# Kernel optimization log

Measured on AMD Instinct MI355X. Metric: run time of the kernel, lower is better.

Reference implementation:

```python
import jax, jax.numpy as jnp
import numpy as np

B, N, M = 8, 1024, 1024
D, H, P = 256, 4, 128
C = D // H  # per-head dim = 64


def setup_inputs() -> dict:
    key = jax.random.key(0)
    ks = jax.random.split(key, 12)
    s = 1.0 / np.sqrt(D)
    return {
        "input_q": jax.random.normal(ks[0], (B, N, D), jnp.float32),
        "input_k": jax.random.normal(ks[1], (B, M, D), jnp.float32),
        "input_v": jax.random.normal(ks[2], (B, M, D), jnp.float32),
        "Wq": jax.random.normal(ks[3], (D, D), jnp.float32) * s,
        "bq": jnp.zeros((D,), jnp.float32),
        "Wk": jax.random.normal(ks[4], (D, D), jnp.float32) * s,
        "bk": jnp.zeros((D,), jnp.float32),
        "Wv": jax.random.normal(ks[5], (D, D), jnp.float32) * s,
        "bv": jnp.zeros((D,), jnp.float32),
        "emb_table": jax.random.normal(ks[6], (P, D), jnp.float32) * s,
        "attention_factors": jax.random.uniform(ks[7], (B, N, M), jnp.float32),
        "emb_indices_qk": jax.random.randint(ks[8], (B, N, M), 0, P, jnp.int32),
        "key_masks": jnp.zeros((B, M), jnp.bool_),
    }


def _split_heads(x):
    # (B, L, D) -> (B, H, L, C)
    b, l, _ = x.shape
    return x.reshape(b, l, H, C).transpose(0, 2, 1, 3)


def reference(input_q, input_k, input_v, Wq, bq, Wk, bk, Wv, bv,
              emb_table, attention_factors, emb_indices_qk, key_masks):
    q = _split_heads(input_q @ Wq.T + bq)  # (B,H,N,C)
    k = _split_heads(input_k @ Wk.T + bk)  # (B,H,M,C)
    v = _split_heads(input_v @ Wv.T + bv)  # (B,H,M,C)

    # embedding bank: (P, D) -> (H, P, C)   ['p (h c) -> h p c']
    emb_bank = emb_table.reshape(P, H, C).transpose(1, 0, 2)
    scores_p_all = jnp.einsum('bhnc,hpc->bhnp', q, emb_bank)  # (B,H,N,P)
    idx = jnp.broadcast_to(emb_indices_qk[:, None], (q.shape[0], H) + emb_indices_qk.shape[1:])
    scores_p = jnp.take_along_axis(scores_p_all, idx, axis=-1)  # (B,H,N,M)

    scores_e = jnp.einsum('bhnc,bhmc->bhnm', q, k)
    scores = (scores_e + scores_p) / jnp.sqrt(jnp.float32(C))
    scores = attention_factors[:, None] * scores
    scores = jnp.where(key_masks[:, None, None, :], -jnp.inf, scores)
    attn = jax.nn.softmax(scores, axis=-1)  # (B,H,N,M)

    hidden = jnp.einsum('bhnm,bhmc->bhnc', attn, v)
    b, h, n, c = hidden.shape
    hidden = hidden.transpose(0, 2, 1, 3).reshape(b, n, h * c)  # (B,N,D)
    return hidden, attn
```

## Files before the change

kernel.cpp:

```cpp
#include <hip/hip_runtime.h>
#include <math.h>

#define Bb 8
#define Nn 1024
#define Mm 1024
#define Dd 256
#define Hh 4
#define Pp 128

using f16x8 = __attribute__((ext_vector_type(8))) _Float16;
using f32x4 = __attribute__((ext_vector_type(4))) float;
using i32x4 = __attribute__((ext_vector_type(4))) int;

#define MFMA16(a, b, c) __builtin_amdgcn_mfma_f32_16x16x32_f16(a, b, c, 0, 0, 0)

__device__ __forceinline__ int swz(int row, int colByte) {
    return row * 128 + (colByte ^ ((row & 7) << 4));
}

__device__ __forceinline__ void stage8_f32(const float* __restrict__ g, unsigned char* dst) {
    f32x4 a = *(const f32x4*)g;
    f32x4 b = *(const f32x4*)(g + 4);
    f16x8 h;
    h[0] = (_Float16)a[0]; h[1] = (_Float16)a[1]; h[2] = (_Float16)a[2]; h[3] = (_Float16)a[3];
    h[4] = (_Float16)b[0]; h[5] = (_Float16)b[1]; h[6] = (_Float16)b[2]; h[7] = (_Float16)b[3];
    *(f16x8*)dst = h;
}

__global__ __launch_bounds__(256) void proj_kernel(
    const float* __restrict__ xq, const float* __restrict__ xk, const float* __restrict__ xv,
    const float* __restrict__ wq, const float* __restrict__ wk, const float* __restrict__ wv,
    const float* __restrict__ bq, const float* __restrict__ bk, const float* __restrict__ bv,
    _Float16* __restrict__ Qo, _Float16* __restrict__ Ko, _Float16* __restrict__ Vt)
{
    __shared__ __align__(16) unsigned char smem[16384];
    unsigned char* aT = smem;
    unsigned char* bT = smem + 8192;

    const int z = blockIdx.z;
    const float* X    = (z == 0) ? xq : (z == 1) ? xk : xv;
    const float* W    = (z == 0) ? wq : (z == 1) ? wk : wv;
    const float* bias = (z == 0) ? bq : (z == 1) ? bk : bv;

    const int r0 = blockIdx.x * 64;
    const int c0 = blockIdx.y * 64;
    const int l = threadIdx.x;
    const int lane = l & 63;
    const int wx = l >> 6;
    const int grp = lane >> 4, col16 = lane & 15;

    f32x4 acc[4] = {};

    for (int kc = 0; kc < 4; ++kc) {
        for (int it = 0; it < 2; ++it) {
            int s = l + it * 256;
            int row = s >> 3, sl = s & 7;
            stage8_f32(X + (size_t)(r0 + row) * Dd + kc * 64 + sl * 8, aT + swz(row, sl * 16));
            stage8_f32(W + (size_t)(c0 + row) * Dd + kc * 64 + sl * 8, bT + swz(row, sl * 16));
        }
        __syncthreads();
        const int arow = wx * 16 + col16;
        f16x8 af0 = *(const f16x8*)(aT + swz(arow, grp * 16));
        f16x8 af1 = *(const f16x8*)(aT + swz(arow, grp * 16 + 64));
#pragma unroll
        for (int t = 0; t < 4; ++t) {
            int brow = t * 16 + col16;
            f16x8 bf0 = *(const f16x8*)(bT + swz(brow, grp * 16));
            f16x8 bf1 = *(const f16x8*)(bT + swz(brow, grp * 16 + 64));
            acc[t] = MFMA16(af0, bf0, acc[t]);
            acc[t] = MFMA16(af1, bf1, acc[t]);
        }
        __syncthreads();
    }

    if (z < 2) {
        _Float16* O = (z == 0) ? Qo : Ko;
        const float osc = (z == 0) ? 0.125f : 1.0f;
#pragma unroll
        for (int t = 0; t < 4; ++t) {
            float bsc = bias[c0 + t * 16 + col16];
#pragma unroll
            for (int j = 0; j < 4; ++j) {
                int r = r0 + wx * 16 + grp * 4 + j;
                O[(size_t)r * Dd + c0 + t * 16 + col16] = (_Float16)((acc[t][j] + bsc) * osc);
            }
        }
    } else {
        _Float16* vt = (_Float16*)smem;
        __syncthreads();
#pragma unroll
        for (int t = 0; t < 4; ++t) {
            float bsc = bias[c0 + t * 16 + col16];
#pragma unroll
            for (int j = 0; j < 4; ++j) {
                int r = wx * 16 + grp * 4 + j;
                int c = t * 16 + col16;
                vt[c * 72 + r] = (_Float16)(acc[t][j] + bsc);
            }
        }
        __syncthreads();
        const int bo = r0 >> 10, m0 = r0 & 1023, h = blockIdx.y;
        for (int it = 0; it < 2; ++it) {
            int s = l + it * 256;
            int c = s >> 3, m8 = s & 7;
            i32x4 val = *(const i32x4*)(vt + c * 72 + m8 * 8);
            *(i32x4*)(Vt + (size_t)((bo * Hh + h) * 64 + c) * Mm + m0 + m8 * 8) = val;
        }
    }
}

__global__ __launch_bounds__(256) void attn_kernel(
    const _Float16* __restrict__ Qi, const _Float16* __restrict__ Ki,
    const _Float16* __restrict__ Vt, const float* __restrict__ emb,
    const float* __restrict__ afac, const int* __restrict__ eidx,
    const unsigned char* __restrict__ kmask,
    float* __restrict__ hid, float* __restrict__ attn)
{
    __shared__ __align__(16) unsigned char smem[63744];
    unsigned char* Uk = smem;
    unsigned char* Uv = smem + 8192;
    unsigned char* Up = smem + 16384;
    _Float16*      spL = (_Float16*)(smem + 24576);
    float*         afT = (float*)(smem + 41984);
    unsigned char* eiT = smem + 59392;

    const int n0 = blockIdx.x * 64;
    const int h = blockIdx.y, b = blockIdx.z;
    const int l = threadIdx.x, lane = l & 63, wx = l >> 6;
    const int grp = lane >> 4, col16 = lane & 15;

    for (int it = 0; it < 2; ++it) {
        int s = l + it * 256, row = s >> 3, sl = s & 7;
        i32x4 v = *(const i32x4*)(Qi + (size_t)(b * Nn + n0 + row) * Dd + h * 64 + sl * 8);
        *(i32x4*)(Uk + swz(row, sl * 16)) = v;
    }
    for (int it = 0; it < 4; ++it) {
        int s = l + it * 256, p = s >> 3, sl = s & 7;
        unsigned char* dst = (p < 64) ? (Uv + swz(p, sl * 16)) : (Up + swz(p - 64, sl * 16));
        stage8_f32(emb + (size_t)p * Dd + h * 64 + sl * 8, dst);
    }
    __syncthreads();

    const int qrow = wx * 16 + col16;
    f16x8 qf0 = *(const f16x8*)(Uk + swz(qrow, grp * 16));
    f16x8 qf1 = *(const f16x8*)(Uk + swz(qrow, grp * 16 + 64));

#pragma unroll
    for (int t = 0; t < 8; ++t) {
        int prow = t * 16 + col16;
        const unsigned char* base = (t < 4) ? Uv : Up;
        int pr = (t < 4) ? prow : prow - 64;
        f16x8 e0 = *(const f16x8*)(base + swz(pr, grp * 16));
        f16x8 e1 = *(const f16x8*)(base + swz(pr, grp * 16 + 64));
        f32x4 a = {};
        a = MFMA16(qf0, e0, a);
        a = MFMA16(qf1, e1, a);
#pragma unroll
        for (int j = 0; j < 4; ++j)
            spL[(wx * 16 + grp * 4 + j) * 136 + t * 16 + col16] = (_Float16)a[j];
    }
    __syncthreads();

    const size_t afrow0 = (size_t)b * Nn * Mm + (size_t)n0 * Mm;
    const _Float16* Kb = Ki + (size_t)b * Mm * Dd + h * 64;
    const _Float16* Vb = Vt + (size_t)((b * Hh + h) * 64) * Mm;

    float sum_[4] = {0.f, 0.f, 0.f, 0.f};

    for (int mt = 0; mt < 16; ++mt) {
        for (int it = 0; it < 2; ++it) {
            int s = l + it * 256, row = s >> 3, sl = s & 7;
            i32x4 v = *(const i32x4*)(Kb + (size_t)(mt * 64 + row) * Dd + sl * 8);
            *(i32x4*)(Uk + swz(row, sl * 16)) = v;
        }
        for (int it = 0; it < 4; ++it) {
            int s = l + it * 256, row = s >> 4, q4 = s & 15;
            size_t g = afrow0 + (size_t)row * Mm + mt * 64 + q4 * 4;
            f32x4 av = *(const f32x4*)(afac + g);
            *(f32x4*)((unsigned char*)afT + row * 272 + q4 * 16) = av;
            i32x4 iv = *(const i32x4*)(eidx + g);
            unsigned int pk = (unsigned)(iv[0] & 255) | ((unsigned)(iv[1] & 255) << 8)
                            | ((unsigned)(iv[2] & 255) << 16) | ((unsigned)(iv[3] & 255) << 24);
            *(unsigned int*)(eiT + row * 68 + q4 * 4) = pk;
        }
        __syncthreads();

        f32x4 sc[4];
#pragma unroll
        for (int t = 0; t < 4; ++t) {
            int krow = t * 16 + col16;
            f16x8 k0 = *(const f16x8*)(Uk + swz(krow, grp * 16));
            f16x8 k1 = *(const f16x8*)(Uk + swz(krow, grp * 16 + 64));
            f32x4 a = {};
            a = MFMA16(qf0, k0, a);
            a = MFMA16(qf1, k1, a);
            sc[t] = a;
        }
#pragma unroll
        for (int t = 0; t < 4; ++t) {
            int m = t * 16 + col16;
            unsigned char mk = kmask[b * Mm + mt * 64 + m];
#pragma unroll
            for (int j = 0; j < 4; ++j) {
                int rl = wx * 16 + grp * 4 + j;
                float sp = (float)spL[rl * 136 + eiT[rl * 68 + m]];
                float s = (sc[t][j] + sp) * afT[rl * 68 + m];
                sum_[j] += mk ? 0.f : __expf(s);
            }
        }
        __syncthreads();
    }

    float rinv[4];
#pragma unroll
    for (int j = 0; j < 4; ++j) {
        float s_ = sum_[j];
#pragma unroll
        for (int d = 1; d < 16; d <<= 1) s_ += __shfl_xor(s_, d, 16);
        rinv[j] = (s_ > 0.f) ? (1.f / s_) : 0.f;
    }

    f32x4 pv[4] = {};
    float* attnB = attn + (size_t)((b * Hh + h) * Nn + n0) * Mm;
    for (int mt = 0; mt < 16; ++mt) {
        for (int it = 0; it < 2; ++it) {
            int s = l + it * 256, row = s >> 3, sl = s & 7;
            i32x4 kv = *(const i32x4*)(Kb + (size_t)(mt * 64 + row) * Dd + sl * 8);
            *(i32x4*)(Uk + swz(row, sl * 16)) = kv;
            i32x4 vv = *(const i32x4*)(Vb + (size_t)row * Mm + mt * 64 + sl * 8);
            *(i32x4*)(Uv + swz(row, sl * 16)) = vv;
        }
        for (int it = 0; it < 4; ++it) {
            int s = l + it * 256, row = s >> 4, q4 = s & 15;
            size_t g = afrow0 + (size_t)row * Mm + mt * 64 + q4 * 4;
            f32x4 av = *(const f32x4*)(afac + g);
            *(f32x4*)((unsigned char*)afT + row * 272 + q4 * 16) = av;
            i32x4 iv = *(const i32x4*)(eidx + g);
            unsigned int pk = (unsigned)(iv[0] & 255) | ((unsigned)(iv[1] & 255) << 8)
                            | ((unsigned)(iv[2] & 255) << 16) | ((unsigned)(iv[3] & 255) << 24);
            *(unsigned int*)(eiT + row * 68 + q4 * 4) = pk;
        }
        __syncthreads();

        f32x4 sc[4];
#pragma unroll
        for (int t = 0; t < 4; ++t) {
            int krow = t * 16 + col16;
            f16x8 k0 = *(const f16x8*)(Uk + swz(krow, grp * 16));
            f16x8 k1 = *(const f16x8*)(Uk + swz(krow, grp * 16 + 64));
            f32x4 a = {};
            a = MFMA16(qf0, k0, a);
            a = MFMA16(qf1, k1, a);
            sc[t] = a;
        }
#pragma unroll
        for (int t = 0; t < 4; ++t) {
            int m = t * 16 + col16;
            unsigned char mk = kmask[b * Mm + mt * 64 + m];
#pragma unroll
            for (int j = 0; j < 4; ++j) {
                int rl = wx * 16 + grp * 4 + j;
                float sp = (float)spL[rl * 136 + eiT[rl * 68 + m]];
                float s = (sc[t][j] + sp) * afT[rl * 68 + m];
                float p = mk ? 0.f : __expf(s) * rinv[j];
                *(_Float16*)(Up + swz(rl, m * 2)) = (_Float16)p;
            }
        }
        __syncthreads();

        const int prow = wx * 16 + col16;
        f16x8 pf0 = *(const f16x8*)(Up + swz(prow, grp * 16));
        f16x8 pf1 = *(const f16x8*)(Up + swz(prow, grp * 16 + 64));
#pragma unroll
        for (int t = 0; t < 4; ++t) {
            int vrow = t * 16 + col16;
            f16x8 v0 = *(const f16x8*)(Uv + swz(vrow, grp * 16));
            f16x8 v1 = *(const f16x8*)(Uv + swz(vrow, grp * 16 + 64));
            pv[t] = MFMA16(pf0, v0, pv[t]);
            pv[t] = MFMA16(pf1, v1, pv[t]);
        }

        {
            const int arow = l >> 2, am0 = (l & 3) * 16;
            f16x8 ph0 = *(const f16x8*)(Up + swz(arow, am0 * 2));
            f16x8 ph1 = *(const f16x8*)(Up + swz(arow, am0 * 2 + 16));
            float* dst = attnB + (size_t)arow * Mm + mt * 64 + am0;
            f32x4 o0 = {(float)ph0[0], (float)ph0[1], (float)ph0[2], (float)ph0[3]};
            f32x4 o1 = {(float)ph0[4], (float)ph0[5], (float)ph0[6], (float)ph0[7]};
            f32x4 o2 = {(float)ph1[0], (float)ph1[1], (float)ph1[2], (float)ph1[3]};
            f32x4 o3 = {(float)ph1[4], (float)ph1[5], (float)ph1[6], (float)ph1[7]};
            *(f32x4*)dst       = o0;
            *(f32x4*)(dst + 4) = o1;
            *(f32x4*)(dst + 8) = o2;
            *(f32x4*)(dst + 12)= o3;
        }
        __syncthreads();
    }

#pragma unroll
    for (int t = 0; t < 4; ++t)
#pragma unroll
        for (int j = 0; j < 4; ++j) {
            int n = n0 + wx * 16 + grp * 4 + j;
            hid[(size_t)(b * Nn + n) * Dd + h * 64 + t * 16 + col16] = pv[t][j];
        }
}

extern "C" void kernel_launch(void* const* d_in, const int* in_sizes, int n_in,
                              void* d_out, int out_size, void* d_ws, size_t ws_size,
                              hipStream_t stream)
{
    (void)in_sizes; (void)n_in; (void)out_size; (void)ws_size;

    const float* xq   = (const float*)d_in[0];
    const float* xk   = (const float*)d_in[1];
    const float* xv   = (const float*)d_in[2];
    const float* wq   = (const float*)d_in[3];
    const float* bq   = (const float*)d_in[4];
    const float* wk   = (const float*)d_in[5];
    const float* bk   = (const float*)d_in[6];
    const float* wv   = (const float*)d_in[7];
    const float* bv   = (const float*)d_in[8];
    const float* emb  = (const float*)d_in[9];
    const float* afac = (const float*)d_in[10];
    const int*   eidx = (const int*)d_in[11];
    const unsigned char* kmask = (const unsigned char*)d_in[12];

    _Float16* Q  = (_Float16*)d_ws;
    _Float16* K  = Q + (size_t)8192 * 256;
    _Float16* Vt = K + (size_t)8192 * 256;

    float* hid  = (float*)d_out;
    float* attn = hid + (size_t)Bb * Nn * Dd;

    proj_kernel<<<dim3(128, 4, 3), 256, 0, stream>>>(xq, xk, xv, wq, wk, wv,
                                                     bq, bk, bv, Q, K, Vt);
    attn_kernel<<<dim3(16, 4, 8), 256, 0, stream>>>(Q, K, Vt, emb, afac, eidx,
                                                    kmask, hid, attn);
}
```

Baseline: 334.1 us.

## Register-prefetch pipelining, 512-thread attention blocks, and coalesced projection stores

Both kernels now prefetch the next tile's global data into registers while computing on the current shared-memory tile. The attention kernel moves to 512 threads, splitting each 64-key tile between two wave groups, and combines the partial row sums and partial PV accumulators through shared memory. Attention probabilities are written to global memory directly from the fp32 value rather than re-read from fp16 shared memory. The key-mask bits are precomputed once per thread, setprio hints are added around the MFMA sections, and the projection kernel uses 128-row tiles with output staged through shared memory for coalesced stores. These changes aim to hide global-load latency and add parallelism, at the cost of more registers and extra synchronisation.

```diff
diff --git a/kernel.cpp b/kernel.cpp
--- a/kernel.cpp
+++ b/kernel.cpp
@@ -18,98 +18,146 @@
     return row * 128 + (colByte ^ ((row & 7) << 4));
 }
 
+__device__ __forceinline__ f16x8 cvt8(f32x4 a, f32x4 b) {
+    f16x8 h;
+    h[0] = (_Float16)a[0]; h[1] = (_Float16)a[1]; h[2] = (_Float16)a[2]; h[3] = (_Float16)a[3];
+    h[4] = (_Float16)b[0]; h[5] = (_Float16)b[1]; h[6] = (_Float16)b[2]; h[7] = (_Float16)b[3];
+    return h;
+}
+
 __device__ __forceinline__ void stage8_f32(const float* __restrict__ g, unsigned char* dst) {
     f32x4 a = *(const f32x4*)g;
     f32x4 b = *(const f32x4*)(g + 4);
-    f16x8 h;
-    h[0] = (_Float16)a[0]; h[1] = (_Float16)a[1]; h[2] = (_Float16)a[2]; h[3] = (_Float16)a[3];
-    h[4] = (_Float16)b[0]; h[5] = (_Float16)b[1]; h[6] = (_Float16)b[2]; h[7] = (_Float16)b[3];
-    *(f16x8*)dst = h;
-}
-
-__global__ __launch_bounds__(256) void proj_kernel(
+    *(f16x8*)dst = cvt8(a, b);
+}
+
+__global__ __launch_bounds__(256, 3) void proj_kernel(
     const float* __restrict__ xq, const float* __restrict__ xk, const float* __restrict__ xv,
     const float* __restrict__ wq, const float* __restrict__ wk, const float* __restrict__ wv,
     const float* __restrict__ bq, const float* __restrict__ bk, const float* __restrict__ bv,
     _Float16* __restrict__ Qo, _Float16* __restrict__ Ko, _Float16* __restrict__ Vt)
 {
-    __shared__ __align__(16) unsigned char smem[16384];
+    __shared__ __align__(16) unsigned char smem[24576];
     unsigned char* aT = smem;
-    unsigned char* bT = smem + 8192;
+    unsigned char* bT = smem + 16384;
 
     const int z = blockIdx.z;
     const float* X    = (z == 0) ? xq : (z == 1) ? xk : xv;
     const float* W    = (z == 0) ? wq : (z == 1) ? wk : wv;
     const float* bias = (z == 0) ? bq : (z == 1) ? bk : bv;
 
-    const int r0 = blockIdx.x * 64;
+    const int r0 = blockIdx.x * 128;
     const int c0 = blockIdx.y * 64;
     const int l = threadIdx.x;
     const int lane = l & 63;
-    const int wx = l >> 6;
+    const int w = l >> 6;
     const int grp = lane >> 4, col16 = lane & 15;
 
-    f32x4 acc[4] = {};
-
-    for (int kc = 0; kc < 4; ++kc) {
-        for (int it = 0; it < 2; ++it) {
-            int s = l + it * 256;
-            int row = s >> 3, sl = s & 7;
-            stage8_f32(X + (size_t)(r0 + row) * Dd + kc * 64 + sl * 8, aT + swz(row, sl * 16));
-            stage8_f32(W + (size_t)(c0 + row) * Dd + kc * 64 + sl * 8, bT + swz(row, sl * 16));
-        }
-        __syncthreads();
-        const int arow = wx * 16 + col16;
-        f16x8 af0 = *(const f16x8*)(aT + swz(arow, grp * 16));
-        f16x8 af1 = *(const f16x8*)(aT + swz(arow, grp * 16 + 64));
-#pragma unroll
-        for (int t = 0; t < 4; ++t) {
-            int brow = t * 16 + col16;
-            f16x8 bf0 = *(const f16x8*)(bT + swz(brow, grp * 16));
-            f16x8 bf1 = *(const f16x8*)(bT + swz(brow, grp * 16 + 64));
-            acc[t] = MFMA16(af0, bf0, acc[t]);
-            acc[t] = MFMA16(af1, bf1, acc[t]);
-        }
-        __syncthreads();
-    }
+    float bs[4];
+#pragma unroll
+    for (int t = 0; t < 4; ++t) bs[t] = bias[c0 + t * 16 + col16];
+
+    f32x4 acc[2][4] = {};
+    f32x4 aR[4][2], bR[2][2];
+
+#define PROJ_LOAD(kc_) { \
+    for (int it = 0; it < 4; ++it) { \
+        int s = l + it * 256, row = s >> 3, sl = s & 7; \
+        const float* g = X + (size_t)(r0 + row) * Dd + (kc_) * 64 + sl * 8; \
+        aR[it][0] = *(const f32x4*)g; aR[it][1] = *(const f32x4*)(g + 4); \
+    } \
+    for (int it = 0; it < 2; ++it) { \
+        int s = l + it * 256, row = s >> 3, sl = s & 7; \
+        const float* g = W + (size_t)(c0 + row) * Dd + (kc_) * 64 + sl * 8; \
+        bR[it][0] = *(const f32x4*)g; bR[it][1] = *(const f32x4*)(g + 4); \
+    } }
+
+#define PROJ_WRITE() { \
+    for (int it = 0; it < 4; ++it) { \
+        int s = l + it * 256, row = s >> 3, sl = s & 7; \
+        *(f16x8*)(aT + swz(row, sl * 16)) = cvt8(aR[it][0], aR[it][1]); \
+    } \
+    for (int it = 0; it < 2; ++it) { \
+        int s = l + it * 256, row = s >> 3, sl = s & 7; \
+        *(f16x8*)(bT + swz(row, sl * 16)) = cvt8(bR[it][0], bR[it][1]); \
+    } }
+
+#define PROJ_COMPUTE() { \
+    __builtin_amdgcn_s_setprio(1); \
+    _Pragma("unroll") for (int rf = 0; rf < 2; ++rf) { \
+        int arow = w * 32 + rf * 16 + col16; \
+        f16x8 a0 = *(const f16x8*)(aT + swz(arow, grp * 16)); \
+        f16x8 a1 = *(const f16x8*)(aT + swz(arow, grp * 16 + 64)); \
+        _Pragma("unroll") for (int t = 0; t < 4; ++t) { \
+            int brow = t * 16 + col16; \
+            f16x8 b0 = *(const f16x8*)(bT + swz(brow, grp * 16)); \
+            f16x8 b1 = *(const f16x8*)(bT + swz(brow, grp * 16 + 64)); \
+            acc[rf][t] = MFMA16(a0, b0, acc[rf][t]); \
+            acc[rf][t] = MFMA16(a1, b1, acc[rf][t]); \
+        } \
+    } \
+    __builtin_amdgcn_s_setprio(0); }
+
+    PROJ_LOAD(0);
+    PROJ_WRITE();
+    __syncthreads();
+    for (int kc = 0; kc < 3; ++kc) {
+        PROJ_LOAD(kc + 1);
+        PROJ_COMPUTE();
+        __syncthreads();
+        PROJ_WRITE();
+        __syncthreads();
+    }
+    PROJ_COMPUTE();
+    __syncthreads();
 
     if (z < 2) {
         _Float16* O = (z == 0) ? Qo : Ko;
         const float osc = (z == 0) ? 0.125f : 1.0f;
-#pragma unroll
-        for (int t = 0; t < 4; ++t) {
-            float bsc = bias[c0 + t * 16 + col16];
-#pragma unroll
-            for (int j = 0; j < 4; ++j) {
-                int r = r0 + wx * 16 + grp * 4 + j;
-                O[(size_t)r * Dd + c0 + t * 16 + col16] = (_Float16)((acc[t][j] + bsc) * osc);
-            }
-        }
+        _Float16* oT = (_Float16*)smem;
+#pragma unroll
+        for (int rf = 0; rf < 2; ++rf)
+#pragma unroll
+            for (int t = 0; t < 4; ++t)
+#pragma unroll
+                for (int j = 0; j < 4; ++j) {
+                    int r = w * 32 + rf * 16 + grp * 4 + j;
+                    oT[r * 72 + t * 16 + col16] = (_Float16)((acc[rf][t][j] + bs[t]) * osc);
+                }
+        __syncthreads();
+        const int row = l >> 1, half = l & 1;
+        const _Float16* src = oT + row * 72 + half * 32;
+        _Float16* dst = O + (size_t)(r0 + row) * Dd + c0 + half * 32;
+#pragma unroll
+        for (int s = 0; s < 4; ++s)
+            *(f16x8*)(dst + s * 8) = *(const f16x8*)(src + s * 8);
     } else {
         _Float16* vt = (_Float16*)smem;
-        __syncthreads();
-#pragma unroll
-        for (int t = 0; t < 4; ++t) {
-            float bsc = bias[c0 + t * 16 + col16];
-#pragma unroll
-            for (int j = 0; j < 4; ++j) {
-                int r = wx * 16 + grp * 4 + j;
-                int c = t * 16 + col16;
-                vt[c * 72 + r] = (_Float16)(acc[t][j] + bsc);
-            }
-        }
+#pragma unroll
+        for (int rf = 0; rf < 2; ++rf)
+#pragma unroll
+            for (int t = 0; t < 4; ++t)
+#pragma unroll
+                for (int j = 0; j < 4; ++j) {
+                    int r = w * 32 + rf * 16 + grp * 4 + j;
+                    int c = t * 16 + col16;
+                    vt[c * 136 + r] = (_Float16)(acc[rf][t][j] + bs[t]);
+                }
         __syncthreads();
         const int bo = r0 >> 10, m0 = r0 & 1023, h = blockIdx.y;
-        for (int it = 0; it < 2; ++it) {
-            int s = l + it * 256;
-            int c = s >> 3, m8 = s & 7;
-            i32x4 val = *(const i32x4*)(vt + c * 72 + m8 * 8);
-            *(i32x4*)(Vt + (size_t)((bo * Hh + h) * 64 + c) * Mm + m0 + m8 * 8) = val;
-        }
-    }
-}
-
-__global__ __launch_bounds__(256) void attn_kernel(
+        const int c = l >> 2, q = l & 3;
+        const _Float16* src = vt + c * 136 + q * 32;
+        _Float16* dst = Vt + (size_t)((bo * Hh + h) * 64 + c) * Mm + m0 + q * 32;
+#pragma unroll
+        for (int s = 0; s < 4; ++s)
+            *(f16x8*)(dst + s * 8) = *(const f16x8*)(src + s * 8);
+    }
+#undef PROJ_LOAD
+#undef PROJ_WRITE
+#undef PROJ_COMPUTE
+}
+
+__global__ __launch_bounds__(512, 4) void attn_kernel(
     const _Float16* __restrict__ Qi, const _Float16* __restrict__ Ki,
     const _Float16* __restrict__ Vt, const float* __restrict__ emb,
     const float* __restrict__ afac, const int* __restrict__ eidx,
@@ -124,186 +172,228 @@
     float*         afT = (float*)(smem + 41984);
     unsigned char* eiT = smem + 59392;
 
-    const int n0 = blockIdx.x * 64;
-    const int h = blockIdx.y, b = blockIdx.z;
-    const int l = threadIdx.x, lane = l & 63, wx = l >> 6;
+    const int bid = blockIdx.x;
+    const int b = bid & 7;
+    const int h = (bid >> 3) & 3;
+    const int n0 = (bid >> 5) * 64;
+    const int l = threadIdx.x, lane = l & 63, w = l >> 6;
+    const int wrow = w & 3, mhalf = w >> 2;
     const int grp = lane >> 4, col16 = lane & 15;
 
-    for (int it = 0; it < 2; ++it) {
-        int s = l + it * 256, row = s >> 3, sl = s & 7;
+    {
+        int row = l >> 3, sl = l & 7;
         i32x4 v = *(const i32x4*)(Qi + (size_t)(b * Nn + n0 + row) * Dd + h * 64 + sl * 8);
         *(i32x4*)(Uk + swz(row, sl * 16)) = v;
     }
-    for (int it = 0; it < 4; ++it) {
-        int s = l + it * 256, p = s >> 3, sl = s & 7;
+#pragma unroll
+    for (int it = 0; it < 2; ++it) {
+        int s = l + it * 512, p = s >> 3, sl = s & 7;
         unsigned char* dst = (p < 64) ? (Uv + swz(p, sl * 16)) : (Up + swz(p - 64, sl * 16));
         stage8_f32(emb + (size_t)p * Dd + h * 64 + sl * 8, dst);
     }
-    __syncthreads();
-
-    const int qrow = wx * 16 + col16;
+    unsigned kbits = 0;
+    for (int mt = 0; mt < 16; ++mt)
+#pragma unroll
+        for (int t = 0; t < 2; ++t) {
+            int m = mt * 64 + mhalf * 32 + t * 16 + col16;
+            kbits |= (kmask[b * Mm + m] ? 1u : 0u) << (mt * 2 + t);
+        }
+    __syncthreads();
+
+    const int qrow = wrow * 16 + col16;
     f16x8 qf0 = *(const f16x8*)(Uk + swz(qrow, grp * 16));
     f16x8 qf1 = *(const f16x8*)(Uk + swz(qrow, grp * 16 + 64));
 
-#pragma unroll
-    for (int t = 0; t < 8; ++t) {
-        int prow = t * 16 + col16;
-        const unsigned char* base = (t < 4) ? Uv : Up;
-        int pr = (t < 4) ? prow : prow - 64;
-        f16x8 e0 = *(const f16x8*)(base + swz(pr, grp * 16));
-        f16x8 e1 = *(const f16x8*)(base + swz(pr, grp * 16 + 64));
-        f32x4 a = {};
-        a = MFMA16(qf0, e0, a);
-        a = MFMA16(qf1, e1, a);
-#pragma unroll
-        for (int j = 0; j < 4; ++j)
-            spL[(wx * 16 + grp * 4 + j) * 136 + t * 16 + col16] = (_Float16)a[j];
+    {
+        const unsigned char* ebase = mhalf ? Up : Uv;
+#pragma unroll
+        for (int t = 0; t < 4; ++t) {
+            int pr = t * 16 + col16;
+            f16x8 e0 = *(const f16x8*)(ebase + swz(pr, grp * 16));
+            f16x8 e1 = *(const f16x8*)(ebase + swz(pr, grp * 16 + 64));
+            f32x4 a = {};
+            a = MFMA16(qf0, e0, a);
+            a = MFMA16(qf1, e1, a);
+#pragma unroll
+            for (int j = 0; j < 4; ++j)
+                spL[(wrow * 16 + grp * 4 + j) * 136 + mhalf * 64 + t * 16 + col16] = (_Float16)a[j];
+        }
     }
     __syncthreads();
 
     const size_t afrow0 = (size_t)b * Nn * Mm + (size_t)n0 * Mm;
     const _Float16* Kb = Ki + (size_t)b * Mm * Dd + h * 64;
     const _Float16* Vb = Vt + (size_t)((b * Hh + h) * 64) * Mm;
+    float* attnB = attn + (size_t)((b * Hh + h) * Nn + n0) * Mm;
+
+    const int krowS = l >> 3, slS = l & 7;
+
+#define LOADK(i_)  (*(const i32x4*)(Kb + (size_t)((i_) * 64 + krowS) * Dd + slS * 8))
+#define LOADV(i_)  (*(const i32x4*)(Vb + (size_t)krowS * Mm + (i_) * 64 + slS * 8))
+#define WRITEK(r_) { *(i32x4*)(Uk + swz(krowS, slS * 16)) = (r_); }
+#define WRITEV(r_) { *(i32x4*)(Uv + swz(krowS, slS * 16)) = (r_); }
+#define LOADAFEI(i_, afR, eiR) { \
+    for (int it = 0; it < 2; ++it) { \
+        int s = l + it * 512, row = s >> 4, q4 = s & 15; \
+        size_t g = afrow0 + (size_t)row * Mm + (size_t)(i_) * 64 + q4 * 4; \
+        afR[it] = *(const f32x4*)(afac + g); \
+        i32x4 iv = *(const i32x4*)(eidx + g); \
+        eiR[it] = (unsigned)(iv[0] & 255) | ((unsigned)(iv[1] & 255) << 8) \
+                | ((unsigned)(iv[2] & 255) << 16) | ((unsigned)(iv[3] & 255) << 24); \
+    } }
+#define WRITEAFEI(afR, eiR) { \
+    for (int it = 0; it < 2; ++it) { \
+        int s = l + it * 512, row = s >> 4, q4 = s & 15; \
+        *(f32x4*)(afT + row * 68 + q4 * 4) = afR[it]; \
+        *(unsigned*)(eiT + row * 68 + q4 * 4) = eiR[it]; \
+    } }
+
+#define COMPUTE_A(mt_) { \
+    __builtin_amdgcn_s_setprio(1); \
+    f32x4 sc[2]; \
+    _Pragma("unroll") for (int t = 0; t < 2; ++t) { \
+        int krow = mhalf * 32 + t * 16 + col16; \
+        f16x8 k0 = *(const f16x8*)(Uk + swz(krow, grp * 16)); \
+        f16x8 k1 = *(const f16x8*)(Uk + swz(krow, grp * 16 + 64)); \
+        f32x4 a = {}; a = MFMA16(qf0, k0, a); a = MFMA16(qf1, k1, a); sc[t] = a; \
+    } \
+    __builtin_amdgcn_s_setprio(0); \
+    _Pragma("unroll") for (int t = 0; t < 2; ++t) { \
+        int m = mhalf * 32 + t * 16 + col16; \
+        _Pragma("unroll") for (int j = 0; j < 4; ++j) { \
+            int rl = wrow * 16 + grp * 4 + j; \
+            float sp = (float)spL[rl * 136 + eiT[rl * 68 + m]]; \
+            float s = (sc[t][j] + sp) * afT[rl * 68 + m]; \
+            float e = ((kbits >> ((mt_) * 2 + t)) & 1) ? 0.f : __expf(s); \
+            sum_[j] += e; \
+        } } }
+
+#define COMPUTE_B(mt_) { \
+    __builtin_amdgcn_s_setprio(1); \
+    f32x4 sc[2]; \
+    _Pragma("unroll") for (int t = 0; t < 2; ++t) { \
+        int krow = mhalf * 32 + t * 16 + col16; \
+        f16x8 k0 = *(const f16x8*)(Uk + swz(krow, grp * 16)); \
+        f16x8 k1 = *(const f16x8*)(Uk + swz(krow, grp * 16 + 64)); \
+        f32x4 a = {}; a = MFMA16(qf0, k0, a); a = MFMA16(qf1, k1, a); sc[t] = a; \
+    } \
+    __builtin_amdgcn_s_setprio(0); \
+    _Pragma("unroll") for (int t = 0; t < 2; ++t) { \
+        int m = mhalf * 32 + t * 16 + col16; \
+        _Pragma("unroll") for (int j = 0; j < 4; ++j) { \
+            int rl = wrow * 16 + grp * 4 + j; \
+            float sp = (float)spL[rl * 136 + eiT[rl * 68 + m]]; \
+            float s = (sc[t][j] + sp) * afT[rl * 68 + m]; \
+            float e = ((kbits >> ((mt_) * 2 + t)) & 1) ? 0.f : __expf(s); \
+            float p = e * rinv[j]; \
+            attnB[(size_t)rl * Mm + (mt_) * 64 + m] = p; \
+            *(_Float16*)(Up + swz(rl, m * 2)) = (_Float16)p; \
+        } } \
+    asm volatile("s_waitcnt lgkmcnt(0)" ::: "memory"); \
+    __builtin_amdgcn_sched_barrier(0); \
+    __builtin_amdgcn_s_setprio(1); \
+    { const int prow = wrow * 16 + col16; \
+      f16x8 pf = *(const f16x8*)(Up + swz(prow, mhalf * 64 + grp * 16)); \
+      _Pragma("unroll") for (int t = 0; t < 4; ++t) { \
+          int vrow = t * 16 + col16; \
+          f16x8 vf = *(const f16x8*)(Uv + swz(vrow, mhalf * 64 + grp * 16)); \
+          pv[t] = MFMA16(pf, vf, pv[t]); \
+      } } \
+    __builtin_amdgcn_s_setprio(0); }
 
     float sum_[4] = {0.f, 0.f, 0.f, 0.f};
-
-    for (int mt = 0; mt < 16; ++mt) {
-        for (int it = 0; it < 2; ++it) {
-            int s = l + it * 256, row = s >> 3, sl = s & 7;
-            i32x4 v = *(const i32x4*)(Kb + (size_t)(mt * 64 + row) * Dd + sl * 8);
-            *(i32x4*)(Uk + swz(row, sl * 16)) = v;
-        }
-        for (int it = 0; it < 4; ++it) {
-            int s = l + it * 256, row = s >> 4, q4 = s & 15;
-            size_t g = afrow0 + (size_t)row * Mm + mt * 64 + q4 * 4;
-            f32x4 av = *(const f32x4*)(afac + g);
-            *(f32x4*)((unsigned char*)afT + row * 272 + q4 * 16) = av;
-            i32x4 iv = *(const i32x4*)(eidx + g);
-            unsigned int pk = (unsigned)(iv[0] & 255) | ((unsigned)(iv[1] & 255) << 8)
-                            | ((unsigned)(iv[2] & 255) << 16) | ((unsigned)(iv[3] & 255) << 24);
-            *(unsigned int*)(eiT + row * 68 + q4 * 4) = pk;
-        }
-        __syncthreads();
-
-        f32x4 sc[4];
-#pragma unroll
-        for (int t = 0; t < 4; ++t) {
-            int krow = t * 16 + col16;
-            f16x8 k0 = *(const f16x8*)(Uk + swz(krow, grp * 16));
-            f16x8 k1 = *(const f16x8*)(Uk + swz(krow, grp * 16 + 64));
-            f32x4 a = {};
-            a = MFMA16(qf0, k0, a);
-            a = MFMA16(qf1, k1, a);
-            sc[t] = a;
-        }
-#pragma unroll
-        for (int t = 0; t < 4; ++t) {
-            int m = t * 16 + col16;
-            unsigned char mk = kmask[b * Mm + mt * 64 + m];
-#pragma unroll
-            for (int j = 0; j < 4; ++j) {
-                int rl = wx * 16 + grp * 4 + j;
-                float sp = (float)spL[rl * 136 + eiT[rl * 68 + m]];
-                float s = (sc[t][j] + sp) * afT[rl * 68 + m];
-                sum_[j] += mk ? 0.f : __expf(s);
-            }
-        }
+    i32x4 kA, kB, vA, vB;
+    f32x4 afA[2], afB[2];
+    unsigned eiA[2], eiB[2];
+
+    kA = LOADK(0); LOADAFEI(0, afA, eiA);
+    kB = LOADK(1); LOADAFEI(1, afB, eiB);
+    WRITEK(kA); WRITEAFEI(afA, eiA);
+    __syncthreads();
+    for (int mt = 0; mt < 16; mt += 2) {
+        int n2 = (mt + 2 < 16) ? mt + 2 : 15;
+        kA = LOADK(n2); LOADAFEI(n2, afA, eiA);
+        COMPUTE_A(mt);
+        __syncthreads();
+        WRITEK(kB); WRITEAFEI(afB, eiB);
+        __syncthreads();
+        int n3 = (mt + 3 < 16) ? mt + 3 : 15;
+        kB = LOADK(n3); LOADAFEI(n3, afB, eiB);
+        COMPUTE_A(mt + 1);
+        __syncthreads();
+        WRITEK(kA); WRITEAFEI(afA, eiA);
         __syncthreads();
     }
 
     float rinv[4];
-#pragma unroll
-    for (int j = 0; j < 4; ++j) {
-        float s_ = sum_[j];
-#pragma unroll
-        for (int d = 1; d < 16; d <<= 1) s_ += __shfl_xor(s_, d, 16);
-        rinv[j] = (s_ > 0.f) ? (1.f / s_) : 0.f;
+    {
+        float* rs = (float*)Up;
+#pragma unroll
+        for (int j = 0; j < 4; ++j) {
+            float s_ = sum_[j];
+#pragma unroll
+            for (int d = 1; d < 16; d <<= 1) s_ += __shfl_xor(s_, d, 16);
+            if (col16 == 0) rs[mhalf * 64 + wrow * 16 + grp * 4 + j] = s_;
+        }
+        __syncthreads();
+#pragma unroll
+        for (int j = 0; j < 4; ++j) {
+            int rl = wrow * 16 + grp * 4 + j;
+            float tot = rs[rl] + rs[64 + rl];
+            rinv[j] = (tot > 0.f) ? (1.f / tot) : 0.f;
+        }
     }
 
     f32x4 pv[4] = {};
-    float* attnB = attn + (size_t)((b * Hh + h) * Nn + n0) * Mm;
-    for (int mt = 0; mt < 16; ++mt) {
-        for (int it = 0; it < 2; ++it) {
-            int s = l + it * 256, row = s >> 3, sl = s & 7;
-            i32x4 kv = *(const i32x4*)(Kb + (size_t)(mt * 64 + row) * Dd + sl * 8);
-            *(i32x4*)(Uk + swz(row, sl * 16)) = kv;
-            i32x4 vv = *(const i32x4*)(Vb + (size_t)row * Mm + mt * 64 + sl * 8);
-            *(i32x4*)(Uv + swz(row, sl * 16)) = vv;
-        }
-        for (int it = 0; it < 4; ++it) {
-            int s = l + it * 256, row = s >> 4, q4 = s & 15;
-            size_t g = afrow0 + (size_t)row * Mm + mt * 64 + q4 * 4;
-            f32x4 av = *(const f32x4*)(afac + g);
-            *(f32x4*)((unsigned char*)afT + row * 272 + q4 * 16) = av;
-            i32x4 iv = *(const i32x4*)(eidx + g);
-            unsigned int pk = (unsigned)(iv[0] & 255) | ((unsigned)(iv[1] & 255) << 8)
-                            | ((unsigned)(iv[2] & 255) << 16) | ((unsigned)(iv[3] & 255) << 24);
-            *(unsigned int*)(eiT + row * 68 + q4 * 4) = pk;
-        }
-        __syncthreads();
-
-        f32x4 sc[4];
-#pragma unroll
-        for (int t = 0; t < 4; ++t) {
-            int krow = t * 16 + col16;
-            f16x8 k0 = *(const f16x8*)(Uk + swz(krow, grp * 16));
-            f16x8 k1 = *(const f16x8*)(Uk + swz(krow, grp * 16 + 64));
-            f32x4 a = {};
-            a = MFMA16(qf0, k0, a);
-            a = MFMA16(qf1, k1, a);
-            sc[t] = a;
-        }
-#pragma unroll
-        for (int t = 0; t < 4; ++t) {
-            int m = t * 16 + col16;
-            unsigned char mk = kmask[b * Mm + mt * 64 + m];
-#pragma unroll
-            for (int j = 0; j < 4; ++j) {
-                int rl = wx * 16 + grp * 4 + j;
-                float sp = (float)spL[rl * 136 + eiT[rl * 68 + m]];
-                float s = (sc[t][j] + sp) * afT[rl * 68 + m];
-                float p = mk ? 0.f : __expf(s) * rinv[j];
-                *(_Float16*)(Up + swz(rl, m * 2)) = (_Float16)p;
-            }
-        }
-        __syncthreads();
-
-        const int prow = wx * 16 + col16;
-        f16x8 pf0 = *(const f16x8*)(Up + swz(prow, grp * 16));
-        f16x8 pf1 = *(const f16x8*)(Up + swz(prow, grp * 16 + 64));
-#pragma unroll
-        for (int t = 0; t < 4; ++t) {
-            int vrow = t * 16 + col16;
-            f16x8 v0 = *(const f16x8*)(Uv + swz(vrow, grp * 16));
-            f16x8 v1 = *(const f16x8*)(Uv + swz(vrow, grp * 16 + 64));
-            pv[t] = MFMA16(pf0, v0, pv[t]);
-            pv[t] = MFMA16(pf1, v1, pv[t]);
-        }
-
-        {
-            const int arow = l >> 2, am0 = (l & 3) * 16;
-            f16x8 ph0 = *(const f16x8*)(Up + swz(arow, am0 * 2));
-            f16x8 ph1 = *(const f16x8*)(Up + swz(arow, am0 * 2 + 16));
-            float* dst = attnB + (size_t)arow * Mm + mt * 64 + am0;
-            f32x4 o0 = {(float)ph0[0], (float)ph0[1], (float)ph0[2], (float)ph0[3]};
-            f32x4 o1 = {(float)ph0[4], (float)ph0[5], (float)ph0[6], (float)ph0[7]};
-            f32x4 o2 = {(float)ph1[0], (float)ph1[1], (float)ph1[2], (float)ph1[3]};
-            f32x4 o3 = {(float)ph1[4], (float)ph1[5], (float)ph1[6], (float)ph1[7]};
-            *(f32x4*)dst       = o0;
-            *(f32x4*)(dst + 4) = o1;
-            *(f32x4*)(dst + 8) = o2;
-            *(f32x4*)(dst + 12)= o3;
-        }
-        __syncthreads();
-    }
-
-#pragma unroll
-    for (int t = 0; t < 4; ++t)
-#pragma unroll
-        for (int j = 0; j < 4; ++j) {
-            int n = n0 + wx * 16 + grp * 4 + j;
-            hid[(size_t)(b * Nn + n) * Dd + h * 64 + t * 16 + col16] = pv[t][j];
-        }
+    kA = LOADK(0); vA = LOADV(0); LOADAFEI(0, afA, eiA);
+    kB = LOADK(1); vB = LOADV(1); LOADAFEI(1, afB, eiB);
+    WRITEK(kA); WRITEV(vA); WRITEAFEI(afA, eiA);
+    __syncthreads();
+    for (int mt = 0; mt < 16; mt += 2) {
+        int n2 = (mt + 2 < 16) ? mt + 2 : 15;
+        kA = LOADK(n2); vA = LOADV(n2); LOADAFEI(n2, afA, eiA);
+        COMPUTE_B(mt);
+        __syncthreads();
+        WRITEK(kB); WRITEV(vB); WRITEAFEI(afB, eiB);
+        __syncthreads();
+        int n3 = (mt + 3 < 16) ? mt + 3 : 15;
+        kB = LOADK(n3); vB = LOADV(n3); LOADAFEI(n3, afB, eiB);
+        COMPUTE_B(mt + 1);
+        __syncthreads();
+        WRITEK(kA); WRITEV(vA); WRITEAFEI(afA, eiA);
+        __syncthreads();
+    }
+
+    {
+        float* pvx = (float*)smem;
+        if (mhalf == 1) {
+#pragma unroll
+            for (int t = 0; t < 4; ++t)
+#pragma unroll
+                for (int j = 0; j < 4; ++j)
+                    pvx[(wrow * 16 + grp * 4 + j) * 68 + t * 16 + col16] = pv[t][j];
+        }
+        __syncthreads();
+        if (mhalf == 0) {
+#pragma unroll
+            for (int t = 0; t < 4; ++t)
+#pragma unroll
+                for (int j = 0; j < 4; ++j) {
+                    int rl = wrow * 16 + grp * 4 + j;
+                    int n = n0 + rl;
+                    hid[(size_t)(b * Nn + n) * Dd + h * 64 + t * 16 + col16] =
+                        pv[t][j] + pvx[rl * 68 + t * 16 + col16];
+                }
+        }
+    }
+#undef LOADK
+#undef LOADV
+#undef WRITEK
+#undef WRITEV
+#undef LOADAFEI
+#undef WRITEAFEI
+#undef COMPUTE_A
+#undef COMPUTE_B
 }
 
 extern "C" void kernel_launch(void* const* d_in, const int* in_sizes, int n_in,
@@ -333,8 +423,8 @@
     float* hid  = (float*)d_out;
     float* attn = hid + (size_t)Bb * Nn * Dd;
 
-    proj_kernel<<<dim3(128, 4, 3), 256, 0, stream>>>(xq, xk, xv, wq, wk, wv,
-                                                     bq, bk, bv, Q, K, Vt);
-    attn_kernel<<<dim3(16, 4, 8), 256, 0, stream>>>(Q, K, Vt, emb, afac, eidx,
-                                                    kmask, hid, attn);
-}
+    proj_kernel<<<dim3(64, 4, 3), 256, 0, stream>>>(xq, xk, xv, wq, wk, wv,
+                                                    bq, bk, bv, Q, K, Vt);
+    attn_kernel<<<512, 512, 0, stream>>>(Q, K, Vt, emb, afac, eidx,
+                                         kmask, hid, attn);
+}
```

After: 520.0 us. 55.6% more time.
